# Kernel tuning notes

Measured on AMD Instinct MI355X. Metric: run time of the kernel, lower is better.

The kernel has to match this reference:

```python
import jax, jax.numpy as jnp
import numpy as np
from jax import lax

V, E, NL, NS, DC, EX = 32000, 1024, 4, 16, 4, 2
DI = EX * E          # 2048 inner dim
DTR = E // 16        # 64 dt_rank
BSZ, L = 2, 512
EPS = 1e-5


def setup_inputs() -> dict:
    key = jax.random.key(0)
    ks = jax.random.split(key, 12)
    s = 0.02
    emb = jax.random.normal(ks[0], (V, E), jnp.float32) * s
    ln_w = jnp.ones((NL, E), jnp.float32)
    ln_b = jnp.zeros((NL, E), jnp.float32)
    in_proj_w = jax.random.normal(ks[1], (NL, 2 * DI, E), jnp.float32) * s
    conv_w = jax.random.normal(ks[2], (NL, DI, DC), jnp.float32) * 0.1
    conv_b = jnp.zeros((NL, DI), jnp.float32)
    x_proj_w = jax.random.normal(ks[3], (NL, DTR + 2 * NS, DI), jnp.float32) * s
    dt_proj_w = jax.random.normal(ks[4], (NL, DI, DTR), jnp.float32) * s
    dt_proj_b = jax.random.normal(ks[5], (NL, DI), jnp.float32) * 0.1
    # canonical S4D-real init: A[d,n] = n+1  ->  A_log = log(A)
    A_log = jnp.log(jnp.tile(jnp.arange(1, NS + 1, dtype=jnp.float32)[None, None, :], (NL, DI, 1)))
    D_param = jnp.ones((NL, DI), jnp.float32)
    out_proj_w = jax.random.normal(ks[6], (NL, E, DI), jnp.float32) * s
    fln_w = jnp.ones((E,), jnp.float32)
    fln_b = jnp.zeros((E,), jnp.float32)
    input_ids = jax.random.randint(ks[7], (BSZ, L), 0, V, jnp.int64)
    targets = jax.random.randint(ks[8], (BSZ, L), 0, V, jnp.int64)
    return dict(input_ids=input_ids, targets=targets, emb=emb, ln_w=ln_w, ln_b=ln_b,
                in_proj_w=in_proj_w, conv_w=conv_w, conv_b=conv_b, x_proj_w=x_proj_w,
                dt_proj_w=dt_proj_w, dt_proj_b=dt_proj_b, A_log=A_log, D_param=D_param,
                out_proj_w=out_proj_w, fln_w=fln_w, fln_b=fln_b)


def _layer_norm(x, w, b):
    mu = x.mean(-1, keepdims=True)
    var = ((x - mu) ** 2).mean(-1, keepdims=True)
    return (x - mu) * lax.rsqrt(var + EPS) * w + b


def _mamba_block(x, in_w, cw, cb, xw, dtw, dtb, a_log, d_par, ow):
    # x: (B,L,E)
    xz = jnp.einsum('ble,fe->blf', x, in_w)          # (B,L,2*DI)
    u, res = jnp.split(xz, 2, axis=-1)               # each (B,L,DI)
    # causal depthwise conv1d, kernel width DC (left pad DC-1)
    u_pad = jnp.pad(u, ((0, 0), (DC - 1, 0), (0, 0)))
    u_conv = sum(cw[:, k] * u_pad[:, k:k + u.shape[1], :] for k in range(DC))
    u = jax.nn.silu(u_conv + cb)
    x_dbl = jnp.einsum('bld,fd->blf', u, xw)         # (B,L,DTR+2*NS)
    dt = x_dbl[..., :DTR]
    Bm = x_dbl[..., DTR:DTR + NS]                    # (B,L,NS)
    Cm = x_dbl[..., DTR + NS:]                       # (B,L,NS)
    delta = jax.nn.softplus(jnp.einsum('blr,dr->bld', dt, dtw) + dtb)  # (B,L,DI)
    A = -jnp.exp(a_log)                              # (DI,NS)
    dA = jnp.exp(delta[..., None] * A)               # (B,L,DI,NS)
    dBu = delta[..., None] * Bm[:, :, None, :] * u[..., None]

    def step(h, inp):
        dA_t, dBu_t, C_t = inp
        h = dA_t * h + dBu_t                         # (B,DI,NS)
        y = jnp.einsum('bdn,bn->bd', h, C_t)
        return h, y

    h0 = jnp.zeros((x.shape[0], DI, NS), x.dtype)
    _, ys = lax.scan(step, h0, (dA.transpose(1, 0, 2, 3), dBu.transpose(1, 0, 2, 3), Cm.transpose(1, 0, 2)))
    y = ys.transpose(1, 0, 2) + u * d_par            # (B,L,DI)
    y = y * jax.nn.silu(res)
    return jnp.einsum('bld,ed->ble', y, ow)


def reference(input_ids, targets, emb, ln_w, ln_b, in_proj_w, conv_w, conv_b,
              x_proj_w, dt_proj_w, dt_proj_b, A_log, D_param, out_proj_w, fln_w, fln_b):
    x = emb[input_ids]                               # (B,L,E)
    for l in range(NL):
        h = _layer_norm(x, ln_w[l], ln_b[l])
        h = _mamba_block(h, in_proj_w[l], conv_w[l], conv_b[l], x_proj_w[l],
                         dt_proj_w[l], dt_proj_b[l], A_log[l], D_param[l], out_proj_w[l])
        x = x + h
    x = _layer_norm(x, fln_w, fln_b)
    logits = jnp.einsum('ble,ve->blv', x, emb)       # tied lm_head
    logp = jax.nn.log_softmax(logits, axis=-1)
    valid = targets != -1
    safe_t = jnp.where(valid, targets, 0)
    nll = -jnp.take_along_axis(logp, safe_t[..., None], axis=-1)[..., 0]
    loss = jnp.where(valid, nll, 0.0).mean()
    return logits, loss
```

## Files before the change

### kernel.cpp

```cpp
#include <hip/hip_runtime.h>
#include <cstdint>
#include <cstddef>

#define L_SEQ 512
#define NBATCH 2
#define NTOK 1024
#define E_DIM 1024
#define V_DIM 32000
#define DI_DIM 2048
#define NS_DIM 16
#define DTR_DIM 64
#define DC_DIM 4
#define NL_DIM 4
#define NC 8
#define LC (L_SEQ / NC)

typedef __bf16 bf16;
typedef __bf16 bf16x8 __attribute__((ext_vector_type(8)));
typedef __bf16 bf16x4 __attribute__((ext_vector_type(4)));
typedef float  f32x4  __attribute__((ext_vector_type(4)));

__device__ __forceinline__ void gload_lds16(const void* g, void* l)
{
    __builtin_amdgcn_global_load_lds((const __attribute__((address_space(1))) uint32_t*)g,
                                     (__attribute__((address_space(3))) uint32_t*)l, 16, 0, 0);
}

__device__ __forceinline__ float softplusf(float z)
{
    return fmaxf(z, 0.0f) + log1pf(expf(-fabsf(z)));
}

__global__ void cast_f32_to_bf16(const float* __restrict__ in, bf16* __restrict__ out, int n4)
{
    int stride = gridDim.x * blockDim.x;
    for (int i = blockIdx.x * blockDim.x + threadIdx.x; i < n4; i += stride) {
        f32x4 v = ((const f32x4*)in)[i];
        bf16x4 o;
        o[0] = (bf16)v[0]; o[1] = (bf16)v[1]; o[2] = (bf16)v[2]; o[3] = (bf16)v[3];
        ((bf16x4*)out)[i] = o;
    }
}

__global__ void cast3_kernel(const float* __restrict__ a, bf16* __restrict__ oa, int na4,
                             const float* __restrict__ b, bf16* __restrict__ ob, int nb4,
                             const float* __restrict__ c, bf16* __restrict__ oc, int nc4)
{
    int stride = gridDim.x * blockDim.x;
    int tot = na4 + nb4 + nc4;
    for (int i = blockIdx.x * blockDim.x + threadIdx.x; i < tot; i += stride) {
        const float* src; bf16* dst; int k = i;
        if (k < na4) { src = a; dst = oa; }
        else if ((k -= na4) < nb4) { src = b; dst = ob; }
        else { k -= nb4; src = c; dst = oc; }
        f32x4 v = ((const f32x4*)src)[k];
        bf16x4 o;
        o[0] = (bf16)v[0]; o[1] = (bf16)v[1]; o[2] = (bf16)v[2]; o[3] = (bf16)v[3];
        ((bf16x4*)dst)[k] = o;
    }
}

__global__ void embed_kernel(const int* __restrict__ ids, const float* __restrict__ emb,
                             float* __restrict__ x)
{
    int t = blockIdx.x;
    int id = ids[t];
    ((f32x4*)(x + (size_t)t * E_DIM))[threadIdx.x] =
        ((const f32x4*)(emb + (size_t)id * E_DIM))[threadIdx.x];
}

__global__ void ln_kernel(const float* __restrict__ x, const float* __restrict__ w,
                          const float* __restrict__ b, bf16* __restrict__ out)
{
    int t = blockIdx.x;
    int tid = threadIdx.x;
    f32x4 v = ((const f32x4*)(x + (size_t)t * E_DIM))[tid];
    float s  = v[0] + v[1] + v[2] + v[3];
    float sq = v[0]*v[0] + v[1]*v[1] + v[2]*v[2] + v[3]*v[3];
#pragma unroll
    for (int off = 1; off < 64; off <<= 1) { s += __shfl_xor(s, off); sq += __shfl_xor(sq, off); }
    __shared__ float ps[4], pq[4];
    if ((tid & 63) == 0) { ps[tid >> 6] = s; pq[tid >> 6] = sq; }
    __syncthreads();
    float S  = ps[0] + ps[1] + ps[2] + ps[3];
    float SQ = pq[0] + pq[1] + pq[2] + pq[3];
    float mu  = S * (1.0f / E_DIM);
    float var = SQ * (1.0f / E_DIM) - mu * mu;
    float rs  = rsqrtf(var + 1e-5f);
    f32x4 wv = ((const f32x4*)w)[tid];
    f32x4 bv = ((const f32x4*)b)[tid];
    bf16x4 o;
#pragma unroll
    for (int i = 0; i < 4; ++i) o[i] = (bf16)((v[i] - mu) * rs * wv[i] + bv[i]);
    ((bf16x4*)(out + (size_t)t * E_DIM))[tid] = o;
}

template<int BM, int BN, int BK, int MODE, int SK>
__global__ __launch_bounds__(256) void gemm_bt(const bf16* __restrict__ A, const bf16* __restrict__ B,
                                               void* __restrict__ Cv, int K,
                                               int lda, int ldb, int ldc,
                                               const float* __restrict__ bias,
                                               int RB, int CB, int CBpad)
{
    int pid = blockIdx.x;
    int per = RB * CBpad;
    int sk  = pid / per;
    int rem = pid - sk * per;
    int xcd = rem & 7;
    int j   = rem >> 3;
    int cpx = CBpad >> 3;
    int rb  = j % RB;
    int cb  = xcd * cpx + j / RB;
    if (cb >= CB) return;
    int kseg = K / SK;
    int kbeg = sk * kseg;
    int kend = kbeg + kseg;

    __shared__ __align__(16) bf16 As[BM * BK];
    __shared__ __align__(16) bf16 Bs[BN * BK];
    int tid  = threadIdx.x;
    int lane = tid & 63;
    int wid  = tid >> 6;
    int wr = wid >> 1, wc = wid & 1;
    int li = lane & 15, lg = lane >> 4;
    const bf16* Ablk = A + (size_t)(rb * BM) * lda;
    const bf16* Bblk = B + (size_t)(cb * BN) * ldb;
    constexpr int MR   = BM / 32;
    constexpr int NR   = BN / 32;
    constexpr int SEGS = BK / 8;
    constexpr int AOPS = BM * SEGS;
    constexpr int TOT  = (BM + BN) * SEGS;
    f32x4 acc[MR][NR] = {};
    for (int k0 = kbeg; k0 < kend; k0 += BK) {
        __syncthreads();
#pragma unroll
        for (int it = 0; it < TOT / 256; ++it) {
            int wbase = it * 256 + wid * 64;
            int idx   = wbase + lane;
            if (wbase < AOPS) {
                int row = idx / SEGS, seg = idx % SEGS;
                int colb = (seg * 16) ^ ((row & (SEGS - 1)) << 4);
                gload_lds16(Ablk + (size_t)row * lda + k0 + (colb >> 1), As + (size_t)wbase * 8);
            } else {
                int bb  = wbase - AOPS;
                int bi  = bb + lane;
                int row = bi / SEGS, seg = bi % SEGS;
                int colb = (seg * 16) ^ ((row & (SEGS - 1)) << 4);
                gload_lds16(Bblk + (size_t)row * ldb + k0 + (colb >> 1), Bs + (size_t)bb * 8);
            }
        }
        __syncthreads();
#pragma unroll
        for (int kk = 0; kk < BK / 32; ++kk) {
            bf16x8 af[MR], bfr[NR];
#pragma unroll
            for (int m = 0; m < MR; ++m) {
                int rowA = wr * (BM/2) + m * 16 + li;
                int cb2  = (kk * 64 + lg * 16) ^ ((rowA & (SEGS - 1)) << 4);
                af[m] = *(const bf16x8*)((const char*)As + (size_t)rowA * (BK * 2) + cb2);
            }
#pragma unroll
            for (int n = 0; n < NR; ++n) {
                int rowB = wc * (BN/2) + n * 16 + li;
                int cb2  = (kk * 64 + lg * 16) ^ ((rowB & (SEGS - 1)) << 4);
                bfr[n] = *(const bf16x8*)((const char*)Bs + (size_t)rowB * (BK * 2) + cb2);
            }
#pragma unroll
            for (int m = 0; m < MR; ++m)
#pragma unroll
                for (int n = 0; n < NR; ++n)
                    acc[m][n] = __builtin_amdgcn_mfma_f32_16x16x32_bf16(af[m], bfr[n], acc[m][n], 0, 0, 0);
        }
    }
    int row0 = rb * BM + wr * (BM/2);
    int col0 = cb * BN + wc * (BN/2);
    float* Cf = (float*)Cv;
    bf16*  Cb = (bf16*)Cv;
#pragma unroll
    for (int m = 0; m < MR; ++m) {
#pragma unroll
        for (int n = 0; n < NR; ++n) {
            int r = row0 + m * 16 + lg * 4;
            int c = col0 + n * 16 + li;
#pragma unroll
            for (int q = 0; q < 4; ++q) {
                float v = acc[m][n][q];
                if (MODE == 0) {
                    Cf[(size_t)(r + q) * ldc + c] = v;
                } else if (MODE == 2) {
                    Cb[(size_t)(r + q) * ldc + c] = (bf16)softplusf(v + bias[c]);
                } else if (MODE == 4) {
                    Cb[(size_t)(r + q) * ldc + c] = (bf16)v;
                } else if (MODE == 5) {
                    atomicAdd(Cf + (size_t)(r + q) * ldc + c, v);
                }
            }
        }
    }
}

template<int BM, int BN, int BK, int MODE, int SK = 1>
static void launch_gemm(const bf16* A, const bf16* B, void* C, int M, int N, int K,
                        int lda, int ldb, int ldc, const float* bias, hipStream_t stream)
{
    int RB = M / BM;
    int CB = (N + BN - 1) / BN;
    int CBpad = (CB + 7) & ~7;
    gemm_bt<BM, BN, BK, MODE, SK><<<RB * CBpad * SK, 256, 0, stream>>>(A, B, C, K, lda, ldb, ldc,
                                                                       bias, RB, CB, CBpad);
}

__global__ __launch_bounds__(512) void gemm256_logits(const bf16* __restrict__ A,
                                                      const bf16* __restrict__ B,
                                                      float* __restrict__ C)
{
    int pid = blockIdx.x;
    int x = pid & 7, i = pid >> 3;
    int cbq = (x < 5) ? 16 : 15;
    int ci = i >> 2;
    if (ci >= cbq) return;
    int cb = (x < 5) ? x * 16 + ci : 80 + (x - 5) * 15 + ci;
    int rb = i & 3;

    __shared__ __align__(16) bf16 Abuf[2][256 * 64];
    __shared__ __align__(16) bf16 Bbuf[2][256 * 64];
    int tid  = threadIdx.x;
    int lane = tid & 63, wid = tid >> 6;
    int wr = wid >> 2, wc = wid & 3;
    int li = lane & 15, lg = lane >> 4;
    const bf16* Ablk = A + (size_t)(rb * 256) * E_DIM;
    const bf16* Bblk = B + (size_t)(cb * 256) * E_DIM;

    f32x4 acc[8][4] = {};

    auto stage = [&](int buf, int k0) {
#pragma unroll
        for (int sw = 0; sw < 4; ++sw) {
            int wb  = sw * 8192 + wid * 1024;
            int y   = wb + lane * 16;
            int row = y >> 7;
            int colb = (y & 127) ^ ((row & 7) << 4);
            gload_lds16(Ablk + (size_t)row * E_DIM + k0 + (colb >> 1),
                        (char*)Abuf[buf] + wb);
        }
#pragma unroll
        for (int sw = 0; sw < 4; ++sw) {
            int wb  = sw * 8192 + wid * 1024;
            int y   = wb + lane * 16;
            int row = y >> 7;
            int colb = (y & 127) ^ ((row & 7) << 4);
            gload_lds16(Bblk + (size_t)row * E_DIM + k0 + (colb >> 1),
                        (char*)Bbuf[buf] + wb);
        }
    };

    stage(0, 0);
    asm volatile("s_waitcnt vmcnt(0)" ::: "memory");
    __builtin_amdgcn_sched_barrier(0);
    __builtin_amdgcn_s_barrier();
    __builtin_amdgcn_sched_barrier(0);
    int cur = 0;
    for (int t = 0; t < 16; ++t) {
        if (t > 0) {
            __builtin_amdgcn_s_barrier();
            __builtin_amdgcn_sched_barrier(0);
        }
        if (t < 15) {
            stage(cur ^ 1, (t + 1) * 64);
            asm volatile("s_waitcnt vmcnt(8)" ::: "memory");
        } else {
            asm volatile("s_waitcnt vmcnt(0)" ::: "memory");
        }
        __builtin_amdgcn_sched_barrier(0);
        __builtin_amdgcn_s_barrier();
        __builtin_amdgcn_sched_barrier(0);
        const char* Ab = (const char*)Abuf[cur];
        const char* Bb = (const char*)Bbuf[cur];
#pragma unroll
        for (int kk = 0; kk < 2; ++kk) {
            bf16x8 af[8], bfr[4];
#pragma unroll
            for (int m = 0; m < 8; ++m) {
                int row = wr * 128 + m * 16 + li;
                int ab  = (row << 7) + ((kk * 64 + lg * 16) ^ ((row & 7) << 4));
                af[m] = *(const bf16x8*)(Ab + ab);
            }
#pragma unroll
            for (int n = 0; n < 4; ++n) {
                int row = wc * 64 + n * 16 + li;
                int bb  = (row << 7) + ((kk * 64 + lg * 16) ^ ((row & 7) << 4));
                bfr[n] = *(const bf16x8*)(Bb + bb);
            }
            __builtin_amdgcn_s_setprio(1);
#pragma unroll
            for (int m = 0; m < 8; ++m)
#pragma unroll
                for (int n = 0; n < 4; ++n)
                    acc[m][n] = __builtin_amdgcn_mfma_f32_16x16x32_bf16(af[m], bfr[n], acc[m][n], 0, 0, 0);
            __builtin_amdgcn_s_setprio(0);
        }
        cur ^= 1;
    }
    int row0 = rb * 256 + wr * 128;
    int col0 = cb * 256 + wc * 64;
#pragma unroll
    for (int m = 0; m < 8; ++m) {
#pragma unroll
        for (int n = 0; n < 4; ++n) {
            int r = row0 + m * 16 + lg * 4;
            int c = col0 + n * 16 + li;
#pragma unroll
            for (int q = 0; q < 4; ++q)
                C[(size_t)(r + q) * V_DIM + c] = acc[m][n][q];
        }
    }
}

__global__ __launch_bounds__(256) void cxk_kernel(
        const bf16* __restrict__ xz, const float* __restrict__ cw,
        const float* __restrict__ cb, const float* __restrict__ xw,
        float* __restrict__ xdbl, bf16* __restrict__ dt_bf, bf16* __restrict__ u_bf)
{
    int t0  = blockIdx.x * 4;
    int bb  = t0 >> 9;
    int tid = threadIdx.x;
    int f   = tid & 127;
    int ks  = tid >> 7;
    __shared__ __align__(16) float sxz[7][256];
    __shared__ __align__(16) float su[4][256];
    __shared__ float pacc[4][128];
    float acc[4] = {0, 0, 0, 0};
    for (int kc = 0; kc < DI_DIM; kc += 256) {
        __syncthreads();
        if (tid < 224) {
            int row = tid >> 5, c8 = (tid & 31) * 8;
            int tr = t0 - 3 + row;
            float vals[8] = {0, 0, 0, 0, 0, 0, 0, 0};
            if (tr >= bb * L_SEQ) {
                bf16x8 v = *(const bf16x8*)&xz[(size_t)tr * (2 * DI_DIM) + kc + c8];
#pragma unroll
                for (int jj = 0; jj < 8; ++jj) vals[jj] = (float)v[jj];
            }
#pragma unroll
            for (int jj = 0; jj < 8; ++jj) sxz[row][c8 + jj] = vals[jj];
        }
        __syncthreads();
        {
            int c = tid;
            const float* cwp = cw + (size_t)(kc + c) * DC_DIM;
            float w0 = cwp[0], w1 = cwp[1], w2 = cwp[2], w3 = cwp[3];
            float bs = cb[kc + c];
#pragma unroll
            for (int tt = 0; tt < 4; ++tt) {
                float a = bs + w0 * sxz[tt][c] + w1 * sxz[tt + 1][c]
                             + w2 * sxz[tt + 2][c] + w3 * sxz[tt + 3][c];
                float uo = a / (1.0f + __expf(-a));
                su[tt][c] = uo;
                u_bf[(size_t)(t0 + tt) * DI_DIM + kc + c] = (bf16)uo;
            }
        }
        __syncthreads();
        if (f < 96) {
            int kb = ks * 128;
            for (int kk = kb; kk < kb + 128; kk += 4) {
                f32x4 wv = *(const f32x4*)&xw[(size_t)f * DI_DIM + kc + kk];
#pragma unroll
                for (int tt = 0; tt < 4; ++tt) {
                    f32x4 uv = *(f32x4*)&su[tt][kk];
                    acc[tt] += wv[0]*uv[0] + wv[1]*uv[1] + wv[2]*uv[2] + wv[3]*uv[3];
                }
            }
        }
    }
    if (ks == 1 && f < 96) {
#pragma unroll
        for (int tt = 0; tt < 4; ++tt) pacc[tt][f] = acc[tt];
    }
    __syncthreads();
    if (ks == 0 && f < 96) {
#pragma unroll
        for (int tt = 0; tt < 4; ++tt) {
            float v = acc[tt] + pacc[tt][f];
            xdbl[(size_t)(t0 + tt) * 96 + f] = v;
            if (f < 64) dt_bf[(size_t)(t0 + tt) * DTR_DIM + f] = (bf16)v;
        }
    }
}

__global__ __launch_bounds__(256) void scan_phase_a(
        const bf16* __restrict__ delta, const float* __restrict__ xdbl,
        const bf16* __restrict__ u_bf, const float* __restrict__ A_log,
        float* __restrict__ Pbuf, float* __restrict__ Sbuf)
{
    int tid = threadIdx.x;
    int c   = blockIdx.x & (NC - 1);
    int dblk= (blockIdx.x >> 3) & 127;
    int b   = blockIdx.x >> 10;
    int d0  = dblk << 4;
    int n = tid & 15, dl = tid >> 4;
    int d = d0 + dl;
    float Ac = -expf(A_log[(size_t)d * NS_DIM + n]);
    float h = 0.0f, P = 1.0f;
    __shared__ float s_dlt[32][16], s_u[32][16], s_B[32][16];
    int tt0 = tid >> 4, cc = tid & 15;
    int tbase = b * L_SEQ + c * LC;
    for (int t0 = 0; t0 < LC; t0 += 32) {
        __syncthreads();
#pragma unroll
        for (int jj = 0; jj < 2; ++jj) {
            int tt = jj * 16 + tt0;
            size_t trow = (size_t)(tbase + t0 + tt);
            s_dlt[tt][cc] = (float)delta[trow * DI_DIM + d0 + cc];
            s_u[tt][cc]   = (float)u_bf[trow * DI_DIM + d0 + cc];
            s_B[tt][cc]   = xdbl[trow * 96 + 64 + cc];
        }
        __syncthreads();
#pragma unroll
        for (int t = 0; t < 32; ++t) {
            float dlt = s_dlt[t][dl];
            float dA  = __expf(dlt * Ac);
            h = fmaf(dA, h, dlt * s_B[t][n] * s_u[t][dl]);
            P *= dA;
        }
    }
    size_t oi = (((size_t)(b * NC + c) * DI_DIM) + d) * NS_DIM + n;
    Pbuf[oi] = P;
    Sbuf[oi] = h;
}

__global__ __launch_bounds__(256) void scan_phase_c(
        const bf16* __restrict__ delta, const float* __restrict__ xdbl,
        const bf16* __restrict__ u_bf, const bf16* __restrict__ xz,
        const float* __restrict__ A_log, const float* __restrict__ D_par,
        const float* __restrict__ Pbuf, const float* __restrict__ Sbuf,
        bf16* __restrict__ y)
{
    int tid = threadIdx.x;
    int c   = blockIdx.x & (NC - 1);
    int dblk= (blockIdx.x >> 3) & 127;
    int b   = blockIdx.x >> 10;
    int d0  = dblk << 4;
    int n = tid & 15, dl = tid >> 4;
    int d = d0 + dl;
    float Ac = -expf(A_log[(size_t)d * NS_DIM + n]);
    float Dp = D_par[d];
    float h = 0.0f;
    for (int cp = 0; cp < c; ++cp) {
        size_t oi = (((size_t)(b * NC + cp) * DI_DIM) + d) * NS_DIM + n;
        h = fmaf(Pbuf[oi], h, Sbuf[oi]);
    }
    __shared__ float s_dlt[32][16], s_u[32][16], s_res[32][16], s_B[32][16], s_C[32][16];
    __shared__ bf16  s_y[32][16];
    int tt0 = tid >> 4, cc = tid & 15;
    int tbase = b * L_SEQ + c * LC;
    for (int t0 = 0; t0 < LC; t0 += 32) {
        __syncthreads();
#pragma unroll
        for (int jj = 0; jj < 2; ++jj) {
            int tt = jj * 16 + tt0;
            size_t trow = (size_t)(tbase + t0 + tt);
            s_dlt[tt][cc] = (float)delta[trow * DI_DIM + d0 + cc];
            s_u[tt][cc]   = (float)u_bf[trow * DI_DIM + d0 + cc];
            s_res[tt][cc] = (float)xz[trow * (2 * DI_DIM) + DI_DIM + d0 + cc];
            s_B[tt][cc]   = xdbl[trow * 96 + 64 + cc];
            s_C[tt][cc]   = xdbl[trow * 96 + 80 + cc];
        }
        __syncthreads();
#pragma unroll
        for (int t = 0; t < 32; ++t) {
            float dlt = s_dlt[t][dl];
            float uu  = s_u[t][dl];
            float dA  = __expf(dlt * Ac);
            float dBu = dlt * s_B[t][n] * uu;
            h = fmaf(dA, h, dBu);
            float yp = h * s_C[t][n];
            yp += __shfl_xor(yp, 1);
            yp += __shfl_xor(yp, 2);
            yp += __shfl_xor(yp, 4);
            yp += __shfl_xor(yp, 8);
            if (n == 0) {
                float res = s_res[t][dl];
                float yv  = fmaf(uu, Dp, yp) * (res / (1.0f + __expf(-res)));
                s_y[t][dl] = (bf16)yv;
            }
        }
        __syncthreads();
#pragma unroll
        for (int jj = 0; jj < 2; ++jj) {
            int tt = jj * 16 + tt0;
            size_t trow = (size_t)(tbase + t0 + tt);
            y[trow * DI_DIM + d0 + cc] = s_y[tt][cc];
        }
    }
}

__global__ void lse_nll_kernel(const float* __restrict__ logits, const int* __restrict__ targets,
                               float* __restrict__ lossp)
{
    int t = blockIdx.x, tid = threadIdx.x;
    const f32x4* row = (const f32x4*)(logits + (size_t)t * V_DIM);
    float m = -1e30f, s = 0.0f;
    for (int i = tid; i < V_DIM / 4; i += 256) {
        f32x4 v = row[i];
        float m4 = fmaxf(fmaxf(v[0], v[1]), fmaxf(v[2], v[3]));
        if (m4 > m) { s *= __expf(m - m4); m = m4; }
        s += __expf(v[0] - m) + __expf(v[1] - m) + __expf(v[2] - m) + __expf(v[3] - m);
    }
#pragma unroll
    for (int off = 1; off < 64; off <<= 1) {
        float mo = __shfl_xor(m, off), so = __shfl_xor(s, off);
        float nm = fmaxf(m, mo);
        s = s * __expf(m - nm) + so * __expf(mo - nm);
        m = nm;
    }
    __shared__ float pm[4], ps2[4];
    if ((tid & 63) == 0) { pm[tid >> 6] = m; ps2[tid >> 6] = s; }
    __syncthreads();
    if (tid == 0) {
        float M = fmaxf(fmaxf(pm[0], pm[1]), fmaxf(pm[2], pm[3]));
        float S = ps2[0] * __expf(pm[0] - M) + ps2[1] * __expf(pm[1] - M)
                + ps2[2] * __expf(pm[2] - M) + ps2[3] * __expf(pm[3] - M);
        int tg = targets[t];
        if (tg >= 0) {
            float v = (M + logf(S)) - logits[(size_t)t * V_DIM + tg];
            atomicAdd(lossp, v * (1.0f / NTOK));
        }
    }
}

extern "C" void kernel_launch(void* const* d_in, const int* in_sizes, int n_in,
                              void* d_out, int out_size, void* d_ws, size_t ws_size,
                              hipStream_t stream)
{
    const int*   ids   = (const int*)d_in[0];
    const int*   tgt   = (const int*)d_in[1];
    const float* emb   = (const float*)d_in[2];
    const float* ln_w  = (const float*)d_in[3];
    const float* ln_b  = (const float*)d_in[4];
    const float* inw   = (const float*)d_in[5];
    const float* convw = (const float*)d_in[6];
    const float* convb = (const float*)d_in[7];
    const float* xw    = (const float*)d_in[8];
    const float* dtw   = (const float*)d_in[9];
    const float* dtb   = (const float*)d_in[10];
    const float* alog  = (const float*)d_in[11];
    const float* dpar  = (const float*)d_in[12];
    const float* outw  = (const float*)d_in[13];
    const float* flnw  = (const float*)d_in[14];
    const float* flnb  = (const float*)d_in[15];
    float* logits = (float*)d_out;
    float* lossp  = logits + (size_t)NTOK * V_DIM;

    const size_t INW_L  = (size_t)2 * DI_DIM * E_DIM;
    const size_t OUTW_L = (size_t)E_DIM * DI_DIM;
    const size_t DTW_L  = (size_t)DI_DIM * DTR_DIM;

    char* wsp = (char*)d_ws;
    size_t off = 0;
    auto alloc = [&](size_t bytes) -> void* {
        void* p = wsp + off;
        off += (bytes + 255) & ~(size_t)255;
        return p;
    };
    bf16*  emb_bf  = (bf16*)alloc((size_t)V_DIM * E_DIM * 2);
    float* x       = (float*)alloc((size_t)NTOK * E_DIM * 4);
    bf16*  h_bf    = (bf16*)alloc((size_t)NTOK * E_DIM * 2);
    bf16*  xzb     = (bf16*)alloc((size_t)NTOK * 2 * DI_DIM * 2);
    bf16*  u_bf    = (bf16*)alloc((size_t)NTOK * DI_DIM * 2);
    float* xdbl    = (float*)alloc((size_t)NTOK * 96 * 4);
    bf16*  dt_bf   = (bf16*)alloc((size_t)NTOK * DTR_DIM * 2);
    bf16*  deltab  = (bf16*)alloc((size_t)NTOK * DI_DIM * 2);
    bf16*  y_bf    = (bf16*)alloc((size_t)NTOK * DI_DIM * 2);
    bf16*  xf_bf   = (bf16*)alloc((size_t)NTOK * E_DIM * 2);
    float* Pbuf    = (float*)alloc((size_t)NBATCH * NC * DI_DIM * NS_DIM * 4);
    float* Sbuf    = (float*)alloc((size_t)NBATCH * NC * DI_DIM * NS_DIM * 4);
    size_t base = off;
    size_t big_need = base + (((size_t)NL_DIM * INW_L * 2 + 255) & ~(size_t)255)
                           + (((size_t)NL_DIM * OUTW_L * 2 + 255) & ~(size_t)255)
                           + (((size_t)NL_DIM * DTW_L * 2 + 255) & ~(size_t)255);
    bool big = (big_need <= ws_size);
    bf16* winl; bf16* woutl; bf16* wdtl;
    if (big) {
        winl  = (bf16*)alloc((size_t)NL_DIM * INW_L * 2);
        woutl = (bf16*)alloc((size_t)NL_DIM * OUTW_L * 2);
        wdtl  = (bf16*)alloc((size_t)NL_DIM * DTW_L * 2);
    } else {
        winl  = (bf16*)alloc(INW_L * 2);
        woutl = (bf16*)alloc(OUTW_L * 2);
        wdtl  = (bf16*)alloc(DTW_L * 2);
    }
    if (off > ws_size) return;

    hipMemsetAsync(lossp, 0, sizeof(float), stream);
    {
        int n4 = (int)((size_t)V_DIM * E_DIM / 4);
        cast_f32_to_bf16<<<4096, 256, 0, stream>>>(emb, emb_bf, n4);
    }
    if (big) {
        cast3_kernel<<<4096, 256, 0, stream>>>(
            inw,  winl,  (int)((size_t)NL_DIM * INW_L / 4),
            outw, woutl, (int)((size_t)NL_DIM * OUTW_L / 4),
            dtw,  wdtl,  (int)((size_t)NL_DIM * DTW_L / 4));
    }
    embed_kernel<<<NTOK, 256, 0, stream>>>(ids, emb, x);

    for (int l = 0; l < NL_DIM; ++l) {
        const bf16* wi = big ? winl  + (size_t)l * INW_L  : winl;
        const bf16* wo = big ? woutl + (size_t)l * OUTW_L : woutl;
        const bf16* wd = big ? wdtl  + (size_t)l * DTW_L  : wdtl;
        if (!big) {
            cast3_kernel<<<2048, 256, 0, stream>>>(
                inw  + (size_t)l * INW_L,  winl,  (int)(INW_L / 4),
                outw + (size_t)l * OUTW_L, woutl, (int)(OUTW_L / 4),
                dtw  + (size_t)l * DTW_L,  wdtl,  (int)(DTW_L / 4));
        }
        ln_kernel<<<NTOK, 256, 0, stream>>>(x, ln_w + l * E_DIM, ln_b + l * E_DIM, h_bf);
        launch_gemm<128, 64, 32, 4>(h_bf, wi, xzb, NTOK, 2 * DI_DIM, E_DIM,
                                    E_DIM, E_DIM, 2 * DI_DIM, nullptr, stream);
        cxk_kernel<<<NTOK / 4, 256, 0, stream>>>(
            xzb, convw + (size_t)l * DI_DIM * DC_DIM, convb + (size_t)l * DI_DIM,
            xw + (size_t)l * 96 * DI_DIM, xdbl, dt_bf, u_bf);
        launch_gemm<64, 64, 32, 2>(dt_bf, wd, deltab, NTOK, DI_DIM, DTR_DIM,
                                   DTR_DIM, DTR_DIM, DI_DIM, dtb + (size_t)l * DI_DIM, stream);
        scan_phase_a<<<NBATCH * (DI_DIM / 16) * NC, 256, 0, stream>>>(
            deltab, xdbl, u_bf, alog + (size_t)l * DI_DIM * NS_DIM, Pbuf, Sbuf);
        scan_phase_c<<<NBATCH * (DI_DIM / 16) * NC, 256, 0, stream>>>(
            deltab, xdbl, u_bf, xzb, alog + (size_t)l * DI_DIM * NS_DIM,
            dpar + (size_t)l * DI_DIM, Pbuf, Sbuf, y_bf);
        launch_gemm<128, 128, 32, 5, 4>(y_bf, wo, x, NTOK, E_DIM, DI_DIM,
                                        DI_DIM, DI_DIM, E_DIM, nullptr, stream);
    }
    ln_kernel<<<NTOK, 256, 0, stream>>>(x, flnw, flnb, xf_bf);
    gemm256_logits<<<512, 512, 0, stream>>>(xf_bf, emb_bf, logits);
    lse_nll_kernel<<<NTOK, 256, 0, stream>>>(logits, tgt, lossp);
}
```

Baseline: 841.1 us.

## Double-buffer generic GEMM loads and shrink logits GEMM K-tile to 32

```diff
diff --git a/kernel.cpp b/kernel.cpp
--- a/kernel.cpp
+++ b/kernel.cpp
@@ -95,6 +95,13 @@
     ((bf16x4*)(out + (size_t)t * E_DIM))[tid] = o;
 }
 
+template<int SEGS>
+__device__ __forceinline__ int swz_row(int row)
+{
+    if constexpr (SEGS == 4) return ((row >> 1) & 3) << 4;
+    else                     return (row & 7) << 4;
+}
+
 template<int BM, int BN, int BK, int MODE, int SK>
 __global__ __launch_bounds__(256) void gemm_bt(const bf16* __restrict__ A, const bf16* __restrict__ B,
                                                void* __restrict__ Cv, int K,
@@ -114,10 +121,9 @@
     if (cb >= CB) return;
     int kseg = K / SK;
     int kbeg = sk * kseg;
-    int kend = kbeg + kseg;
-
-    __shared__ __align__(16) bf16 As[BM * BK];
-    __shared__ __align__(16) bf16 Bs[BN * BK];
+
+    __shared__ __align__(16) bf16 As[2][BM * BK];
+    __shared__ __align__(16) bf16 Bs[2][BN * BK];
     int tid  = threadIdx.x;
     int lane = tid & 63;
     int wid  = tid >> 6;
@@ -125,52 +131,73 @@
     int li = lane & 15, lg = lane >> 4;
     const bf16* Ablk = A + (size_t)(rb * BM) * lda;
     const bf16* Bblk = B + (size_t)(cb * BN) * ldb;
-    constexpr int MR   = BM / 32;
-    constexpr int NR   = BN / 32;
-    constexpr int SEGS = BK / 8;
-    constexpr int AOPS = BM * SEGS;
-    constexpr int TOT  = (BM + BN) * SEGS;
+    constexpr int MR     = BM / 32;
+    constexpr int NR     = BN / 32;
+    constexpr int SEGS   = BK / 8;
+    constexpr int AOPS   = BM * SEGS;
+    constexpr int TOT    = (BM + BN) * SEGS;
+    constexpr int WLOADS = TOT / 256;
     f32x4 acc[MR][NR] = {};
-    for (int k0 = kbeg; k0 < kend; k0 += BK) {
-        __syncthreads();
-#pragma unroll
-        for (int it = 0; it < TOT / 256; ++it) {
+
+    auto stage = [&](int buf, int k0) {
+#pragma unroll
+        for (int it = 0; it < WLOADS; ++it) {
             int wbase = it * 256 + wid * 64;
             int idx   = wbase + lane;
             if (wbase < AOPS) {
                 int row = idx / SEGS, seg = idx % SEGS;
-                int colb = (seg * 16) ^ ((row & (SEGS - 1)) << 4);
-                gload_lds16(Ablk + (size_t)row * lda + k0 + (colb >> 1), As + (size_t)wbase * 8);
+                int colb = (seg * 16) ^ swz_row<SEGS>(row);
+                gload_lds16(Ablk + (size_t)row * lda + k0 + (colb >> 1), &As[buf][(size_t)wbase * 8]);
             } else {
                 int bb  = wbase - AOPS;
                 int bi  = bb + lane;
                 int row = bi / SEGS, seg = bi % SEGS;
-                int colb = (seg * 16) ^ ((row & (SEGS - 1)) << 4);
-                gload_lds16(Bblk + (size_t)row * ldb + k0 + (colb >> 1), Bs + (size_t)bb * 8);
-            }
-        }
-        __syncthreads();
+                int colb = (seg * 16) ^ swz_row<SEGS>(row);
+                gload_lds16(Bblk + (size_t)row * ldb + k0 + (colb >> 1), &Bs[buf][(size_t)bb * 8]);
+            }
+        }
+    };
+
+    int NT = kseg / BK;
+    stage(0, kbeg);
+    int cur = 0;
+    for (int t = 0; t < NT; ++t) {
+        if (t + 1 < NT) {
+            stage(cur ^ 1, kbeg + (t + 1) * BK);
+            asm volatile("s_waitcnt vmcnt(%0)" :: "i"(WLOADS) : "memory");
+        } else {
+            asm volatile("s_waitcnt vmcnt(0)" ::: "memory");
+        }
+        __builtin_amdgcn_sched_barrier(0);
+        __builtin_amdgcn_s_barrier();
+        __builtin_amdgcn_sched_barrier(0);
 #pragma unroll
         for (int kk = 0; kk < BK / 32; ++kk) {
             bf16x8 af[MR], bfr[NR];
 #pragma unroll
             for (int m = 0; m < MR; ++m) {
                 int rowA = wr * (BM/2) + m * 16 + li;
-                int cb2  = (kk * 64 + lg * 16) ^ ((rowA & (SEGS - 1)) << 4);
-                af[m] = *(const bf16x8*)((const char*)As + (size_t)rowA * (BK * 2) + cb2);
+                int cb2  = (kk * 64 + lg * 16) ^ swz_row<SEGS>(rowA);
+                af[m] = *(const bf16x8*)((const char*)As[cur] + (size_t)rowA * (BK * 2) + cb2);
             }
 #pragma unroll
             for (int n = 0; n < NR; ++n) {
                 int rowB = wc * (BN/2) + n * 16 + li;
-                int cb2  = (kk * 64 + lg * 16) ^ ((rowB & (SEGS - 1)) << 4);
-                bfr[n] = *(const bf16x8*)((const char*)Bs + (size_t)rowB * (BK * 2) + cb2);
-            }
+                int cb2  = (kk * 64 + lg * 16) ^ swz_row<SEGS>(rowB);
+                bfr[n] = *(const bf16x8*)((const char*)Bs[cur] + (size_t)rowB * (BK * 2) + cb2);
+            }
+            __builtin_amdgcn_s_setprio(1);
 #pragma unroll
             for (int m = 0; m < MR; ++m)
 #pragma unroll
                 for (int n = 0; n < NR; ++n)
                     acc[m][n] = __builtin_amdgcn_mfma_f32_16x16x32_bf16(af[m], bfr[n], acc[m][n], 0, 0, 0);
-        }
+            __builtin_amdgcn_s_setprio(0);
+        }
+        __builtin_amdgcn_sched_barrier(0);
+        __builtin_amdgcn_s_barrier();
+        __builtin_amdgcn_sched_barrier(0);
+        cur ^= 1;
     }
     int row0 = rb * BM + wr * (BM/2);
     int col0 = cb * BN + wc * (BN/2);
@@ -222,8 +249,8 @@
     int cb = (x < 5) ? x * 16 + ci : 80 + (x - 5) * 15 + ci;
     int rb = i & 3;
 
-    __shared__ __align__(16) bf16 Abuf[2][256 * 64];
-    __shared__ __align__(16) bf16 Bbuf[2][256 * 64];
+    __shared__ __align__(16) bf16 Abuf[2][256 * 32];
+    __shared__ __align__(16) bf16 Bbuf[2][256 * 32];
     int tid  = threadIdx.x;
     int lane = tid & 63, wid = tid >> 6;
     int wr = wid >> 2, wc = wid & 3;
@@ -235,39 +262,31 @@
 
     auto stage = [&](int buf, int k0) {
 #pragma unroll
-        for (int sw = 0; sw < 4; ++sw) {
+        for (int sw = 0; sw < 2; ++sw) {
             int wb  = sw * 8192 + wid * 1024;
             int y   = wb + lane * 16;
-            int row = y >> 7;
-            int colb = (y & 127) ^ ((row & 7) << 4);
+            int row = y >> 6;
+            int colb = (y & 63) ^ (((row >> 1) & 3) << 4);
             gload_lds16(Ablk + (size_t)row * E_DIM + k0 + (colb >> 1),
                         (char*)Abuf[buf] + wb);
         }
 #pragma unroll
-        for (int sw = 0; sw < 4; ++sw) {
+        for (int sw = 0; sw < 2; ++sw) {
             int wb  = sw * 8192 + wid * 1024;
             int y   = wb + lane * 16;
-            int row = y >> 7;
-            int colb = (y & 127) ^ ((row & 7) << 4);
+            int row = y >> 6;
+            int colb = (y & 63) ^ (((row >> 1) & 3) << 4);
             gload_lds16(Bblk + (size_t)row * E_DIM + k0 + (colb >> 1),
                         (char*)Bbuf[buf] + wb);
         }
     };
 
     stage(0, 0);
-    asm volatile("s_waitcnt vmcnt(0)" ::: "memory");
-    __builtin_amdgcn_sched_barrier(0);
-    __builtin_amdgcn_s_barrier();
-    __builtin_amdgcn_sched_barrier(0);
     int cur = 0;
-    for (int t = 0; t < 16; ++t) {
-        if (t > 0) {
-            __builtin_amdgcn_s_barrier();
-            __builtin_amdgcn_sched_barrier(0);
-        }
-        if (t < 15) {
-            stage(cur ^ 1, (t + 1) * 64);
-            asm volatile("s_waitcnt vmcnt(8)" ::: "memory");
+    for (int t = 0; t < 32; ++t) {
+        if (t + 1 < 32) {
+            stage(cur ^ 1, (t + 1) * 32);
+            asm volatile("s_waitcnt vmcnt(4)" ::: "memory");
         } else {
             asm volatile("s_waitcnt vmcnt(0)" ::: "memory");
         }
@@ -276,19 +295,18 @@
         __builtin_amdgcn_sched_barrier(0);
         const char* Ab = (const char*)Abuf[cur];
         const char* Bb = (const char*)Bbuf[cur];
-#pragma unroll
-        for (int kk = 0; kk < 2; ++kk) {
+        {
             bf16x8 af[8], bfr[4];
 #pragma unroll
             for (int m = 0; m < 8; ++m) {
                 int row = wr * 128 + m * 16 + li;
-                int ab  = (row << 7) + ((kk * 64 + lg * 16) ^ ((row & 7) << 4));
+                int ab  = (row << 6) + ((lg * 16) ^ (((row >> 1) & 3) << 4));
                 af[m] = *(const bf16x8*)(Ab + ab);
             }
 #pragma unroll
             for (int n = 0; n < 4; ++n) {
                 int row = wc * 64 + n * 16 + li;
-                int bb  = (row << 7) + ((kk * 64 + lg * 16) ^ ((row & 7) << 4));
+                int bb  = (row << 6) + ((lg * 16) ^ (((row >> 1) & 3) << 4));
                 bfr[n] = *(const bf16x8*)(Bb + bb);
             }
             __builtin_amdgcn_s_setprio(1);
@@ -299,6 +317,9 @@
                     acc[m][n] = __builtin_amdgcn_mfma_f32_16x16x32_bf16(af[m], bfr[n], acc[m][n], 0, 0, 0);
             __builtin_amdgcn_s_setprio(0);
         }
+        __builtin_amdgcn_sched_barrier(0);
+        __builtin_amdgcn_s_barrier();
+        __builtin_amdgcn_sched_barrier(0);
         cur ^= 1;
     }
     int row0 = rb * 256 + wr * 128;
```

Measured after the change: 843.1 us. About the same (+0.2%).
